# Kernel optimization log

Hardware: AMD Instinct MI355X
Metric: run time of the kernel (lower is better)

Reference implementation:

```python
import jax, jax.numpy as jnp
import numpy as np


NUM_HEADS = 16


def setup_inputs() -> dict:
    key = jax.random.key(0)
    ks = jax.random.split(key, 6)
    B, Sq, Skv, DQ, DKV = 2, 1024, 4096, 1024, 768
    return {
        "x_q": jax.random.normal(ks[0], (B, Sq, DQ), jnp.float32),
        "x_kv": jax.random.normal(ks[1], (B, Skv, DKV), jnp.float32),
        "Wq": jax.random.normal(ks[2], (DQ, DQ), jnp.float32) * 0.02,
        "Wk": jax.random.normal(ks[3], (DQ, DKV), jnp.float32) * 0.02,
        "Wv": jax.random.normal(ks[4], (DQ, DKV), jnp.float32) * 0.02,
        "Wo": jax.random.normal(ks[5], (DQ, DQ), jnp.float32) * 0.02,
    }


def _split_heads(x):
    # Faithful to torch view(B, H, S, hd): a pure reshape, NOT a transpose.
    B, S, D = x.shape
    return x.reshape(B, NUM_HEADS, S, D // NUM_HEADS)


def reference(x_q, x_kv, Wq, Wk, Wv, Wo):
    head_dim = x_q.shape[-1] // NUM_HEADS
    # torch Linear: y = x @ W.T, weight shape (out, in)
    Q = _split_heads(jnp.einsum("bsd,od->bso", x_q, Wq))   # (B,H,Sq',hd)
    K = _split_heads(jnp.einsum("bsd,od->bso", x_kv, Wk))  # (B,H,Skv',hd)
    V = _split_heads(jnp.einsum("bsd,od->bso", x_kv, Wv))
    # Scale is 1/head_dim (not 1/sqrt), faithful to the source.
    scores = jnp.einsum("bhqd,bhkd->bhqk", Q, K) / head_dim
    attn = jax.nn.softmax(scores, axis=-1)
    out = jnp.einsum("bhqk,bhkd->bhqd", attn, V)  # (B,H,Sq',hd)
    B, Sq, DQ = x_q.shape
    out = out.transpose(0, 2, 1, 3).reshape(B, Sq, DQ)
    return jnp.einsum("bsd,od->bso", out, Wo)
```

## Files before the change

kernel.cpp:

```cpp
#include <hip/hip_runtime.h>
#include <hip/hip_bf16.h>
#include <cstdint>

#define THREADS 256

typedef __attribute__((ext_vector_type(8))) short bf16x8;
typedef __attribute__((ext_vector_type(4))) float f32x4;

__device__ __forceinline__ void load_lds16(const void* g, void* l) {
    __builtin_amdgcn_global_load_lds(
        (const __attribute__((address_space(1))) unsigned int*)g,
        (__attribute__((address_space(3))) unsigned int*)l, 16, 0, 0);
}

__device__ __forceinline__ unsigned short f2bf(float x) {
    __hip_bfloat16 hb = __float2bfloat16(x);
    return *(unsigned short*)&hb;
}

__global__ __launch_bounds__(THREADS)
void cast_inputs(const float* __restrict__ xq, const float* __restrict__ xkv,
                 const float* __restrict__ wq, const float* __restrict__ wk,
                 const float* __restrict__ wv, const float* __restrict__ wo,
                 unsigned short* __restrict__ oq, unsigned short* __restrict__ okv,
                 unsigned short* __restrict__ owq, unsigned short* __restrict__ owk,
                 unsigned short* __restrict__ owv, unsigned short* __restrict__ owo) {
    const unsigned n0 = 524288, n1 = 1572864, n2 = 262144, n3 = 196608, n4 = 196608;
    unsigned i = blockIdx.x * THREADS + threadIdx.x;
    const float* src; unsigned short* dst; unsigned off;
    if (i < n0)                    { src = xq;  dst = oq;  off = i; }
    else if (i < n0+n1)            { src = xkv; dst = okv; off = i - n0; }
    else if (i < n0+n1+n2)         { src = wq;  dst = owq; off = i - n0 - n1; }
    else if (i < n0+n1+n2+n3)      { src = wk;  dst = owk; off = i - n0 - n1 - n2; }
    else if (i < n0+n1+n2+n3+n4)   { src = wv;  dst = owv; off = i - n0 - n1 - n2 - n3; }
    else                           { src = wo;  dst = owo; off = i - n0 - n1 - n2 - n3 - n4; }
    float4 v = *(const float4*)(src + (size_t)off * 4);
    ushort4 o;
    o.x = f2bf(v.x); o.y = f2bf(v.y); o.z = f2bf(v.z); o.w = f2bf(v.w);
    *(ushort4*)(dst + (size_t)off * 4) = o;
}

template <bool OUTF32>
__global__ __launch_bounds__(THREADS)
void gemm_bf16_nt64(const unsigned short* __restrict__ A, const unsigned short* __restrict__ W,
                    void* __restrict__ Cout, int M, int N, int Kd) {
    __shared__ __align__(16) unsigned short As[64 * 64];
    __shared__ __align__(16) unsigned short Bs[64 * 64];

    const int t    = threadIdx.x;
    const int w    = t >> 6;
    const int lane = t & 63;
    const int l15  = lane & 15;
    const int quad = lane >> 4;
    const int wm   = w & 1;
    const int wn   = w >> 1;
    const int bM = blockIdx.y * 64;
    const int bN = blockIdx.x * 64;

    const int srow = t >> 3;
    const int scol = ((t & 7) ^ ((t >> 3) & 7)) << 3;
    const unsigned short* ga = A + (size_t)(bM + srow) * Kd + scol;
    const unsigned short* gb = W + (size_t)(bN + srow) * Kd + scol;
    const int lbase = w * 512;

    int aoff[2][2], boff[2][2];
#pragma unroll
    for (int kk = 0; kk < 2; ++kk)
#pragma unroll
        for (int mt = 0; mt < 2; ++mt) {
            aoff[kk][mt] = (wm * 32 + mt * 16 + l15) * 64 + (((kk * 4 + quad) ^ (l15 & 7)) << 3);
            boff[kk][mt] = (wn * 32 + mt * 16 + l15) * 64 + (((kk * 4 + quad) ^ (l15 & 7)) << 3);
        }

    f32x4 acc[2][2];
#pragma unroll
    for (int mt = 0; mt < 2; ++mt)
#pragma unroll
        for (int nt = 0; nt < 2; ++nt)
#pragma unroll
            for (int r = 0; r < 4; ++r) acc[mt][nt][r] = 0.f;

    for (int k0 = 0; k0 < Kd; k0 += 64) {
        __syncthreads();
#pragma unroll
        for (int it = 0; it < 2; ++it) {
            load_lds16(ga + (size_t)it * 32 * Kd + k0, &As[lbase + it * 2048]);
            load_lds16(gb + (size_t)it * 32 * Kd + k0, &Bs[lbase + it * 2048]);
        }
        __syncthreads();

#pragma unroll
        for (int kk = 0; kk < 2; ++kk) {
            bf16x8 af[2], bf[2];
#pragma unroll
            for (int mt = 0; mt < 2; ++mt) af[mt] = *(const bf16x8*)&As[aoff[kk][mt]];
#pragma unroll
            for (int nt = 0; nt < 2; ++nt) bf[nt] = *(const bf16x8*)&Bs[boff[kk][nt]];
#pragma unroll
            for (int mt = 0; mt < 2; ++mt)
#pragma unroll
                for (int nt = 0; nt < 2; ++nt)
                    acc[mt][nt] = __builtin_amdgcn_mfma_f32_16x16x32_bf16(af[mt], bf[nt], acc[mt][nt], 0, 0, 0);
        }
    }

#pragma unroll
    for (int mt = 0; mt < 2; ++mt)
#pragma unroll
        for (int r = 0; r < 4; ++r) {
            int row = bM + wm * 32 + mt * 16 + quad * 4 + r;
            int col = bN + wn * 32 + l15;
            if (OUTF32) {
                float* cp = (float*)Cout + (size_t)row * N + col;
#pragma unroll
                for (int nt = 0; nt < 2; ++nt) cp[nt * 16] = acc[mt][nt][r];
            } else {
                unsigned short* cp = (unsigned short*)Cout + (size_t)row * N + col;
#pragma unroll
                for (int nt = 0; nt < 2; ++nt) cp[nt * 16] = f2bf(acc[mt][nt][r]);
            }
        }
}

__global__ __launch_bounds__(THREADS)
void gemm_bf16_kvt(const unsigned short* __restrict__ A, const unsigned short* __restrict__ W,
                   unsigned short* __restrict__ Kn, unsigned short* __restrict__ Vt,
                   int M, int Kd) {
    __shared__ __align__(16) unsigned short As[128 * 64];
    __shared__ __align__(16) unsigned short Bs[128 * 64];

    const int t    = threadIdx.x;
    const int w    = t >> 6;
    const int lane = t & 63;
    const int l15  = lane & 15;
    const int quad = lane >> 4;
    const int wm   = w & 1;
    const int wn   = w >> 1;
    const int bM = blockIdx.y * 128;
    const int bN = blockIdx.x * 128;

    const int srow = t >> 3;
    const int scol = ((t & 7) ^ ((t >> 4) & 7)) << 3;
    const unsigned short* ga = A + (size_t)(bM + srow) * Kd + scol;
    const unsigned short* gb = W + (size_t)(bN + srow) * Kd + scol;
    const int lbase = w * 512;

    const int xr = (l15 >> 1) & 7;
    int aoff[2][4], boff[2][4];
#pragma unroll
    for (int kk = 0; kk < 2; ++kk)
#pragma unroll
        for (int mt = 0; mt < 4; ++mt) {
            aoff[kk][mt] = (wm * 64 + mt * 16 + l15) * 64 + (((kk * 4 + quad) ^ xr) << 3);
            boff[kk][mt] = (wn * 64 + mt * 16 + l15) * 64 + (((kk * 4 + quad) ^ xr) << 3);
        }

    f32x4 acc[4][4];
#pragma unroll
    for (int mt = 0; mt < 4; ++mt)
#pragma unroll
        for (int nt = 0; nt < 4; ++nt)
#pragma unroll
            for (int r = 0; r < 4; ++r) acc[mt][nt][r] = 0.f;

    for (int k0 = 0; k0 < Kd; k0 += 64) {
        __syncthreads();
#pragma unroll
        for (int it = 0; it < 4; ++it) {
            load_lds16(ga + (size_t)it * 32 * Kd + k0, &As[lbase + it * 2048]);
            load_lds16(gb + (size_t)it * 32 * Kd + k0, &Bs[lbase + it * 2048]);
        }
        __syncthreads();

#pragma unroll
        for (int kk = 0; kk < 2; ++kk) {
            bf16x8 af[4], bf[4];
#pragma unroll
            for (int mt = 0; mt < 4; ++mt) af[mt] = *(const bf16x8*)&As[aoff[kk][mt]];
#pragma unroll
            for (int nt = 0; nt < 4; ++nt) bf[nt] = *(const bf16x8*)&Bs[boff[kk][nt]];
#pragma unroll
            for (int mt = 0; mt < 4; ++mt)
#pragma unroll
                for (int nt = 0; nt < 4; ++nt)
                    acc[mt][nt] = __builtin_amdgcn_mfma_f32_16x16x32_bf16(af[mt], bf[nt], acc[mt][nt], 0, 0, 0);
        }
    }

    const int rbase = bM + wm * 64;
    const int b  = rbase >> 12;
    const int h  = (rbase & 4095) >> 8;
    if (bN < 1024) {
        const int G = (bN + wn * 64) >> 6;
        unsigned short* kp = Kn + (size_t)(b * 16 + h) * 262144 + (size_t)G * 256 * 64 + l15;
#pragma unroll
        for (int mt = 0; mt < 4; ++mt)
#pragma unroll
            for (int r = 0; r < 4; ++r) {
                int u = (rbase & 255) + mt * 16 + quad * 4 + r;
                unsigned short* cp = kp + (size_t)u * 64;
#pragma unroll
                for (int nt = 0; nt < 4; ++nt) cp[nt * 16] = f2bf(acc[mt][nt][r]);
            }
    } else {
        const int Gv = (bN - 1024 + wn * 64) >> 6;
        unsigned short* vp = Vt + (size_t)(b * 16 + h) * 262144 + (size_t)Gv * 256;
#pragma unroll
        for (int nt = 0; nt < 4; ++nt) {
            int d = nt * 16 + l15;
#pragma unroll
            for (int mt = 0; mt < 4; ++mt) {
                int u = (rbase & 255) + mt * 16 + quad * 4;
                ushort4 pk;
                pk.x = f2bf(acc[mt][nt][0]);
                pk.y = f2bf(acc[mt][nt][1]);
                pk.z = f2bf(acc[mt][nt][2]);
                pk.w = f2bf(acc[mt][nt][3]);
                *(ushort4*)(vp + (size_t)d * 4096 + u) = pk;
            }
        }
    }
}

__global__ __launch_bounds__(THREADS, 2)
void attn_mfma6(const unsigned short* __restrict__ Q, const unsigned short* __restrict__ K,
                const unsigned short* __restrict__ Vt, unsigned short* __restrict__ AO) {
    extern __shared__ __align__(16) unsigned short sm[];
    unsigned short* Ks = sm;
    unsigned short* Vs = sm + 8192;
    unsigned short* Ps = sm + 16384;
    float* OS = (float*)sm;
    float* Lw = (float*)(sm + 26624);

    const int bid  = blockIdx.x;
    const int slot = bid >> 3;
    const int qq   = slot & 15;
    const int hh   = (bid & 7) + 8 * (slot >> 4);
    const int q0 = qq * 64;
    const int h  = hh & 15;
    const int b  = hh >> 4;

    const int t    = threadIdx.x;
    const int w    = t >> 6;
    const int lane = t & 63;
    const int l15  = lane & 15;
    const int quad = lane >> 4;

    const unsigned short* Qh = Q + (size_t)b * 1048576 + (size_t)h * 65536 + (size_t)q0 * 64;
    const unsigned short* Kh = K + (size_t)b * 4194304 + (size_t)h * 262144;
    const unsigned short* Vh = Vt + (size_t)(b * 16 + h) * 262144;

    bf16x8 Qb[4][2];
#pragma unroll
    for (int qt = 0; qt < 4; ++qt)
#pragma unroll
        for (int kk = 0; kk < 2; ++kk)
            Qb[qt][kk] = *(const bf16x8*)(Qh + (size_t)(qt * 16 + l15) * 64 + kk * 32 + quad * 8);

    const unsigned short* gK = Kh + (size_t)(t >> 3) * 64 + (((t & 7) ^ ((t >> 3) & 7)) << 3);
    const unsigned short* gV = Vh + (size_t)(t >> 4) * 4096 + (((t & 15) ^ ((t >> 4) & 7)) << 3);
    const int lb = w * 512;

    int koff[2][2];
#pragma unroll
    for (int kvt = 0; kvt < 2; ++kvt)
#pragma unroll
        for (int kk = 0; kk < 2; ++kk)
            koff[kvt][kk] = (w * 32 + kvt * 16 + l15) * 64 + (((kk * 4 + quad) ^ (l15 & 7)) << 3);
    int voff[4];
#pragma unroll
    for (int dt = 0; dt < 4; ++dt)
        voff[dt] = (dt * 16 + l15) * 128 + (((w * 4 + quad) ^ (l15 & 7)) << 3);

    const int pw  = w * 2560;
    const int pq  = pw + l15 * 40;

    f32x4 Oacc[4][4];
#pragma unroll
    for (int qt = 0; qt < 4; ++qt)
#pragma unroll
        for (int dt = 0; dt < 4; ++dt)
#pragma unroll
            for (int r = 0; r < 4; ++r) Oacc[qt][dt][r] = 0.f;
    float lsum[4] = {0.f, 0.f, 0.f, 0.f};

    const float scale = 1.0f / 64.0f;

    for (int kc = 0; kc < 32; ++kc) {
        __syncthreads();
#pragma unroll
        for (int it = 0; it < 4; ++it)
            load_lds16(gK + (size_t)kc * 8192 + it * 2048, &Ks[lb + it * 2048]);
#pragma unroll
        for (int it = 0; it < 4; ++it)
            load_lds16(gV + (size_t)kc * 128 + (size_t)it * 65536, &Vs[lb + it * 2048]);
        __syncthreads();

#pragma unroll
        for (int kvt = 0; kvt < 2; ++kvt) {
            bf16x8 ka = *(const bf16x8*)&Ks[koff[kvt][0]];
            bf16x8 kb = *(const bf16x8*)&Ks[koff[kvt][1]];
#pragma unroll
            for (int qt = 0; qt < 4; ++qt) {
                f32x4 S = {0.f, 0.f, 0.f, 0.f};
                S = __builtin_amdgcn_mfma_f32_16x16x32_bf16(ka, Qb[qt][0], S, 0, 0, 0);
                S = __builtin_amdgcn_mfma_f32_16x16x32_bf16(kb, Qb[qt][1], S, 0, 0, 0);
                float p0 = __expf(S[0] * scale);
                float p1 = __expf(S[1] * scale);
                float p2 = __expf(S[2] * scale);
                float p3 = __expf(S[3] * scale);
                lsum[qt] += (p0 + p1) + (p2 + p3);
                ushort4 pk4;
                pk4.x = f2bf(p0); pk4.y = f2bf(p1); pk4.z = f2bf(p2); pk4.w = f2bf(p3);
                *(ushort4*)&Ps[pq + qt * 640 + kvt * 16 + quad * 4] = pk4;
            }
        }
        asm volatile("s_waitcnt lgkmcnt(0)" ::: "memory");

        bf16x8 Vf[4];
#pragma unroll
        for (int dt = 0; dt < 4; ++dt) Vf[dt] = *(const bf16x8*)&Vs[voff[dt]];
#pragma unroll
        for (int qt = 0; qt < 4; ++qt) {
            bf16x8 Pa = *(const bf16x8*)&Ps[pq + qt * 640 + quad * 8];
#pragma unroll
            for (int dt = 0; dt < 4; ++dt)
                Oacc[qt][dt] = __builtin_amdgcn_mfma_f32_16x16x32_bf16(Pa, Vf[dt], Oacc[qt][dt], 0, 0, 0);
        }
    }

#pragma unroll
    for (int qt = 0; qt < 4; ++qt) {
        float v = lsum[qt];
        v += __shfl_xor(v, 16);
        v += __shfl_xor(v, 32);
        lsum[qt] = v;
    }
    __syncthreads();
    if (lane < 16) {
#pragma unroll
        for (int qt = 0; qt < 4; ++qt)
            Lw[w * 64 + qt * 16 + lane] = lsum[qt];
    }
    if (w > 0) {
        float* myOS = OS + (w - 1) * 4352;
#pragma unroll
        for (int qt = 0; qt < 4; ++qt)
#pragma unroll
            for (int dt = 0; dt < 4; ++dt)
                *(f32x4*)&myOS[(dt * 16 + l15) * 68 + qt * 16 + quad * 4] = Oacc[qt][dt];
    }
    __syncthreads();
    if (w == 0) {
#pragma unroll
        for (int qt = 0; qt < 4; ++qt) {
            f32x4 lv = *(const f32x4*)&Lw[qt * 16 + quad * 4];
            lv += *(const f32x4*)&Lw[64 + qt * 16 + quad * 4];
            lv += *(const f32x4*)&Lw[128 + qt * 16 + quad * 4];
            lv += *(const f32x4*)&Lw[192 + qt * 16 + quad * 4];
            f32x4 inv;
#pragma unroll
            for (int r = 0; r < 4; ++r) inv[r] = 1.0f / lv[r];
#pragma unroll
            for (int dt = 0; dt < 4; ++dt) {
                f32x4 o = Oacc[qt][dt];
                int os = (dt * 16 + l15) * 68 + qt * 16 + quad * 4;
                o += *(const f32x4*)&OS[os];
                o += *(const f32x4*)&OS[4352 + os];
                o += *(const f32x4*)&OS[8704 + os];
#pragma unroll
                for (int r = 0; r < 4; ++r) {
                    int q = qt * 16 + quad * 4 + r;
                    AO[(size_t)b * 1048576 + (size_t)(q0 + q) * 1024 + (h << 6) + dt * 16 + l15]
                        = f2bf(o[r] * inv[r]);
                }
            }
        }
    }
}

extern "C" void kernel_launch(void* const* d_in, const int* in_sizes, int n_in,
                              void* d_out, int out_size, void* d_ws, size_t ws_size,
                              hipStream_t stream) {
    const float* x_q  = (const float*)d_in[0];
    const float* x_kv = (const float*)d_in[1];
    const float* Wq   = (const float*)d_in[2];
    const float* Wk   = (const float*)d_in[3];
    const float* Wv   = (const float*)d_in[4];
    const float* Wo   = (const float*)d_in[5];
    float* out = (float*)d_out;

    unsigned short* base   = (unsigned short*)d_ws;
    unsigned short* xq_bf  = base;
    unsigned short* xkv_bf = base + 2097152;
    unsigned short* wq_bf  = base + 8388608;
    unsigned short* wk_bf  = base + 9437184;
    unsigned short* wv_bf  = base + 10223616;
    unsigned short* wo_bf  = base + 11010048;
    unsigned short* Qw     = base + 12058624;
    unsigned short* Kw     = base + 14155776;
    unsigned short* AOb    = base + 22544384;
    unsigned short* Vtw    = base + 30932992;

    dim3 blk(THREADS);
    cast_inputs<<<dim3(11776), blk, 0, stream>>>(x_q, x_kv, Wq, Wk, Wv, Wo,
                                                 xq_bf, xkv_bf, wq_bf, wk_bf, wv_bf, wo_bf);
    gemm_bf16_nt64<false><<<dim3(16, 32), blk, 0, stream>>>(xq_bf, wq_bf, (void*)Qw, 2048, 1024, 1024);
    gemm_bf16_kvt<<<dim3(16, 64), blk, 0, stream>>>(xkv_bf, wk_bf, Kw, Vtw, 8192, 768);
    attn_mfma6<<<dim3(512), blk, 54272, stream>>>(Qw, Kw, Vtw, AOb);
    gemm_bf16_nt64<true><<<dim3(16, 32), blk, 0, stream>>>(AOb, wo_bf, (void*)out, 2048, 1024, 1024);
}
```

Before: 218.2 us.

## Split attention KV range across two blocks and combine partials in separate kernel

The attention kernel now splits the 4096-key loop into two halves handled by separate blocks, doubling the grid to 1024 blocks. Each block writes unnormalised fp32 partial outputs and row sums to the workspace, and a new combine kernel sums the halves, normalises and casts to bf16. Launch bounds go from 2 to 3 blocks per CU and LDS shrinks slightly, so the intent is better occupancy and load balance across the 256 CUs. The cost is an extra kernel launch and fp32 partial traffic. The partials reuse workspace that held the already-consumed casted inputs. No running max is shown, so summing the halves presumably relies on the softmax being unshifted.

Result: slower. 233.7 us (+7.1%).

```diff
diff --git a/kernel.cpp b/kernel.cpp
--- a/kernel.cpp
+++ b/kernel.cpp
@@ -222,20 +222,23 @@
     }
 }
 
-__global__ __launch_bounds__(THREADS, 2)
-void attn_mfma6(const unsigned short* __restrict__ Q, const unsigned short* __restrict__ K,
-                const unsigned short* __restrict__ Vt, unsigned short* __restrict__ AO) {
+__global__ __launch_bounds__(THREADS, 3)
+void attn_mfma7(const unsigned short* __restrict__ Q, const unsigned short* __restrict__ K,
+                const unsigned short* __restrict__ Vt, float* __restrict__ Op,
+                float* __restrict__ Lp) {
     extern __shared__ __align__(16) unsigned short sm[];
     unsigned short* Ks = sm;
     unsigned short* Vs = sm + 8192;
     unsigned short* Ps = sm + 16384;
     float* OS = (float*)sm;
-    float* Lw = (float*)(sm + 26624);
+    float* Lw = (float*)(sm + 26112);
 
     const int bid  = blockIdx.x;
     const int slot = bid >> 3;
-    const int qq   = slot & 15;
-    const int hh   = (bid & 7) + 8 * (slot >> 4);
+    const int hh   = (bid & 7) + 8 * (slot >> 5);
+    const int rem  = slot & 31;
+    const int qq   = rem >> 1;
+    const int half = rem & 1;
     const int q0 = qq * 64;
     const int h  = hh & 15;
     const int b  = hh >> 4;
@@ -286,7 +289,7 @@
 
     const float scale = 1.0f / 64.0f;
 
-    for (int kc = 0; kc < 32; ++kc) {
+    for (int kc = half * 16; kc < half * 16 + 16; ++kc) {
         __syncthreads();
 #pragma unroll
         for (int it = 0; it < 4; ++it)
@@ -358,9 +361,13 @@
             lv += *(const f32x4*)&Lw[64 + qt * 16 + quad * 4];
             lv += *(const f32x4*)&Lw[128 + qt * 16 + quad * 4];
             lv += *(const f32x4*)&Lw[192 + qt * 16 + quad * 4];
-            f32x4 inv;
-#pragma unroll
-            for (int r = 0; r < 4; ++r) inv[r] = 1.0f / lv[r];
+            if (l15 == 0) {
+#pragma unroll
+                for (int r = 0; r < 4; ++r) {
+                    int q = qt * 16 + quad * 4 + r;
+                    Lp[(size_t)half * 32768 + ((size_t)b * 1024 + q0 + q) * 16 + h] = lv[r];
+                }
+            }
 #pragma unroll
             for (int dt = 0; dt < 4; ++dt) {
                 f32x4 o = Oacc[qt][dt];
@@ -371,12 +378,30 @@
 #pragma unroll
                 for (int r = 0; r < 4; ++r) {
                     int q = qt * 16 + quad * 4 + r;
-                    AO[(size_t)b * 1048576 + (size_t)(q0 + q) * 1024 + (h << 6) + dt * 16 + l15]
-                        = f2bf(o[r] * inv[r]);
+                    Op[(size_t)half * 2097152 + ((size_t)b * 1024 + q0 + q) * 1024
+                       + (h << 6) + dt * 16 + l15] = o[r];
                 }
             }
         }
     }
+}
+
+__global__ __launch_bounds__(THREADS)
+void combine_o(const float* __restrict__ Op, const float* __restrict__ Lp,
+               unsigned short* __restrict__ AO) {
+    unsigned i = blockIdx.x * THREADS + threadIdx.x;
+    unsigned flat = i * 4;
+    unsigned bq = flat >> 10;
+    unsigned h  = (flat & 1023) >> 6;
+    float4 o0 = *(const float4*)(Op + flat);
+    float4 o1 = *(const float4*)(Op + 2097152 + flat);
+    float inv = 1.0f / (Lp[bq * 16 + h] + Lp[32768 + bq * 16 + h]);
+    ushort4 o;
+    o.x = f2bf((o0.x + o1.x) * inv);
+    o.y = f2bf((o0.y + o1.y) * inv);
+    o.z = f2bf((o0.z + o1.z) * inv);
+    o.w = f2bf((o0.w + o1.w) * inv);
+    *(ushort4*)(AO + flat) = o;
 }
 
 extern "C" void kernel_launch(void* const* d_in, const int* in_sizes, int n_in,
@@ -400,13 +425,16 @@
     unsigned short* Qw     = base + 12058624;
     unsigned short* Kw     = base + 14155776;
     unsigned short* AOb    = base + 22544384;
+    float*          Lp     = (float*)(base + 24641536);
     unsigned short* Vtw    = base + 30932992;
+    float*          Opf    = (float*)d_ws;
 
     dim3 blk(THREADS);
     cast_inputs<<<dim3(11776), blk, 0, stream>>>(x_q, x_kv, Wq, Wk, Wv, Wo,
                                                  xq_bf, xkv_bf, wq_bf, wk_bf, wv_bf, wo_bf);
     gemm_bf16_nt64<false><<<dim3(16, 32), blk, 0, stream>>>(xq_bf, wq_bf, (void*)Qw, 2048, 1024, 1024);
     gemm_bf16_kvt<<<dim3(16, 64), blk, 0, stream>>>(xkv_bf, wk_bf, Kw, Vtw, 8192, 768);
-    attn_mfma6<<<dim3(512), blk, 54272, stream>>>(Qw, Kw, Vtw, AOb);
+    attn_mfma7<<<dim3(1024), blk, 53248, stream>>>(Qw, Kw, Vtw, Opf, Lp);
+    combine_o<<<dim3(2048), blk, 0, stream>>>(Opf, Lp, AOb);
     gemm_bf16_nt64<true><<<dim3(16, 32), blk, 0, stream>>>(AOb, wo_bf, (void*)out, 2048, 1024, 1024);
 }
```
